# Optimization experiments

Hardware: AMD Instinct MI355X
Metric: run time of the kernel (lower is better)

The kernel has to match this reference:

```python
import jax, jax.numpy as jnp
import numpy as np
from jax import lax

NPOINT = 1024
FG_NSAMPLE = 512
TOPK = 2048
NSAMPLE = 32
RADIUS = 0.3
BN_EPS = 1e-5


def masked_fps(xyz, mask, n):
    """Farthest point sampling restricted to points where mask is True.
    xyz: [B,N,3] (grad-stopped), mask: [B,N] bool. Returns int32 [B,n] indices.
    Equivalent to running FPS on the masked subset starting at its first point."""
    xyz = lax.stop_gradient(xyz)

    def one(x, m):
        mind0 = jnp.where(m, jnp.float32(1e10), jnp.float32(-1.0))

        def body(i, carry):
            mind, idxs = carry
            sel = jnp.argmax(mind).astype(jnp.int32)
            d = jnp.sum((x - x[sel]) ** 2, axis=-1)
            mind = jnp.where(m, jnp.minimum(mind, d), jnp.float32(-1.0))
            return mind, idxs.at[i].set(sel)

        _, idxs = lax.fori_loop(0, n, body, (mind0, jnp.zeros((n,), jnp.int32)))
        return idxs

    return jax.vmap(one)(xyz, mask)


def ball_query(xyz, new_xyz, radius, nsample):
    """xyz: [B,N,3], new_xyz: [B,S,3] -> int32 [B,S,nsample] of first neighbors
    within radius (padded with the first found index, as in pointnet2 CUDA)."""
    x = lax.stop_gradient(xyz)
    q = lax.stop_gradient(new_xyz)
    d2 = jnp.sum((q[:, :, None, :] - x[:, None, :, :]) ** 2, axis=-1)  # [B,S,N]
    N = x.shape[1]
    ar = jnp.arange(N, dtype=jnp.float32)
    key = jnp.where(d2 <= radius * radius, ar, jnp.float32(N))
    neg_top, _ = lax.top_k(-key, nsample)  # smallest nsample indices
    idx = (-neg_top).astype(jnp.int32)
    first = idx[..., :1]
    idx = jnp.where(idx >= N, first, idx)
    return jnp.clip(idx, 0, N - 1)


def conv_bn_relu_2d(x, W, g, b):
    # x: [B,C,S,ns], W: [O,C]; 1x1 conv (no bias) + training-mode BN + ReLU
    y = jnp.einsum('oc,bcsn->bosn', W, x)
    mu = y.mean((0, 2, 3), keepdims=True)
    var = y.var((0, 2, 3), keepdims=True)
    y = (y - mu) * lax.rsqrt(var + BN_EPS) * g[None, :, None, None] + b[None, :, None, None]
    return jax.nn.relu(y)


def conv_bn_relu_1d(x, W, g, b):
    # x: [B,C,N]
    y = jnp.einsum('oc,bcn->bon', W, x)
    mu = y.mean((0, 2), keepdims=True)
    var = y.var((0, 2), keepdims=True)
    y = (y - mu) * lax.rsqrt(var + BN_EPS) * g[None, :, None] + b[None, :, None]
    return jax.nn.relu(y)


def batch_gather_points(x, idx):
    # x: [B,N,3], idx: [B,...] -> [B,...,3]
    return jax.vmap(lambda a, i: a[i])(x, idx)


def batch_gather_feats(f, idx):
    # f: [B,C,N], idx: [B,S,ns] -> [B,C,S,ns]
    return jax.vmap(lambda a, i: a[:, i])(f, idx)


def setup_inputs() -> dict:
    key = jax.random.key(0)
    ks = jax.random.split(key, 16)
    B, N, C = 4, 16384, 128
    s = 0.05
    return {
        'xyz': jax.random.uniform(ks[0], (B, N, 3), dtype=jnp.float32),
        'features': jax.random.normal(ks[1], (B, C, N), dtype=jnp.float32),
        # grouped shared MLP: (3+C)->128->128->256
        'w1': jax.random.normal(ks[2], (128, 131), dtype=jnp.float32) * s,
        'g1': jnp.ones((128,), jnp.float32), 'b1': jnp.zeros((128,), jnp.float32),
        'w2': jax.random.normal(ks[3], (128, 128), dtype=jnp.float32) * s,
        'g2': jnp.ones((128,), jnp.float32), 'b2': jnp.zeros((128,), jnp.float32),
        'w3': jax.random.normal(ks[4], (256, 128), dtype=jnp.float32) * s,
        'g3': jnp.ones((256,), jnp.float32), 'b3': jnp.zeros((256,), jnp.float32),
        # fbs mask MLP: C->64->2 (last layer plain conv with bias)
        'fw1': jax.random.normal(ks[5], (64, 128), dtype=jnp.float32) * s,
        'fg1': jnp.ones((64,), jnp.float32), 'fb1': jnp.zeros((64,), jnp.float32),
        'fw2': jax.random.normal(ks[6], (2, 64), dtype=jnp.float32) * s,
        'fbias2': jnp.zeros((2,), jnp.float32),
    }


def reference(xyz, features, w1, g1, b1, w2, g2, b2, w3, g3, b3, fw1, fg1, fb1, fw2, fbias2):
    B, N, _ = xyz.shape
    # --- FBS: foreground/background scoring ---
    h = conv_bn_relu_1d(features, fw1, fg1, fb1)                 # [B,64,N]
    mask_scores = jnp.einsum('oc,bcn->bon', fw2, h) + fbias2[None, :, None]  # [B,2,N]
    soft = jax.nn.softmax(mask_scores, axis=1)
    margin = soft[:, 1, :] - soft[:, 0, :]                        # [B,N]
    _, top_idx = lax.top_k(margin, TOPK)
    fg_mask = jnp.zeros((B, N), bool).at[jnp.arange(B)[:, None], top_idx].set(True)
    # --- mask-restricted FPS on foreground and background ---
    fg_idx = masked_fps(xyz, fg_mask, FG_NSAMPLE)                 # [B,512]
    bg_idx = masked_fps(xyz, ~fg_mask, NPOINT - FG_NSAMPLE)       # [B,512]
    indices = jnp.concatenate([fg_idx, bg_idx], axis=1)          # [B,npoint]
    new_xyz = batch_gather_points(xyz, indices)                   # [B,npoint,3]
    # --- ball query + grouping ---
    idx = ball_query(xyz, new_xyz, RADIUS, NSAMPLE)               # [B,S,ns]
    grouped_xyz = batch_gather_points(xyz, idx)                   # [B,S,ns,3]
    grouped_xyz = grouped_xyz - new_xyz[:, :, None, :]
    grouped_xyz = jnp.transpose(grouped_xyz, (0, 3, 1, 2))        # [B,3,S,ns]
    grouped_feats = batch_gather_feats(features, idx)             # [B,C,S,ns]
    x = jnp.concatenate([grouped_xyz, grouped_feats], axis=1)     # [B,3+C,S,ns]
    # --- shared MLP + max pool over neighbors ---
    x = conv_bn_relu_2d(x, w1, g1, b1)
    x = conv_bn_relu_2d(x, w2, g2, b2)
    x = conv_bn_relu_2d(x, w3, g3, b3)
    new_features = jnp.max(x, axis=-1)                            # [B,256,S]
    return new_xyz, new_features, indices, mask_scores
```

## Files before the change

kernel.cpp:

```cpp
#include <hip/hip_runtime.h>

#define BB 4
#define NPT 16384
#define CIN 128
#define SS 1024
#define NS 32
#define PP 131072
#define TOPKK 2048

typedef unsigned short u16;
typedef unsigned int u32;
typedef unsigned long long u64;
typedef float v2 __attribute__((ext_vector_type(2)));
typedef short bf16x8 __attribute__((ext_vector_type(8)));
typedef float f32x4 __attribute__((ext_vector_type(4)));

__device__ __forceinline__ float bf2f(u32 v){ return __uint_as_float(v << 16); }
__device__ __forceinline__ u16 f2bf(float f){
  u32 u = __float_as_uint(f);
  u32 r = (u + 0x7FFFu + ((u >> 16) & 1u)) >> 16;
  return (u16)r;
}
__device__ __forceinline__ u32 keyOf(float m){
  u32 u = __float_as_uint(m);
  return (u & 0x80000000u) ? ~u : (u | 0x80000000u);
}

__device__ __forceinline__ float wave_max_f32(float v){
  #define STEP(CTRL) { int o_ = __builtin_amdgcn_update_dpp(0, __float_as_int(v), CTRL, 0xf, 0xf, true); \
                       v = fmaxf(v, __int_as_float(o_)); }
  STEP(0x111) STEP(0x112) STEP(0x114) STEP(0x118)
  STEP(0x142) STEP(0x143)
  #undef STEP
  return __int_as_float(__builtin_amdgcn_readlane(__float_as_int(v), 63));
}

__device__ __forceinline__ float row_max16(float v){
  #define STEP(CTRL) { int o_ = __builtin_amdgcn_update_dpp(0, __float_as_int(v), CTRL, 0xf, 0xf, true); \
                       v = fmaxf(v, __int_as_float(o_)); }
  STEP(0x111) STEP(0x112) STEP(0x114) STEP(0x118)
  #undef STEP
  return v;
}

#define OFF_NEWXYZ 0ull
#define OFF_MARGIN 49152ull
#define OFF_FGMASK 311296ull
#define OFF_IDXNB  573440ull
#define OFF_MSTAT  1097728ull
#define OFF_SSA    1098240ull
#define OFF_WT0    1104384ull
#define OFF_W1B    1137152ull
#define OFF_W2B    1178112ull
#define OFF_W3B    1210880ull
#define OFF_MPART  1407488ull
#define OFF_CPART  2456064ull
#define OFF_REGB   10844672ull
#define OFF_REGA   44399104ull
#define WS_NEED    86342144ull

__global__ void k_prep(const float* __restrict__ w1, const float* __restrict__ w2,
                       const float* __restrict__ w3, const float* __restrict__ fw1,
                       float* __restrict__ wt0, u16* __restrict__ w1b, u16* __restrict__ w2b,
                       u16* __restrict__ w3b){
  int gt = blockIdx.x*blockDim.x + threadIdx.x;
  int gs = gridDim.x*blockDim.x;
  for (int i = gt; i < 128*64;  i += gs){ int k=i>>6, m=i&63;  wt0[i] = fw1[m*128+k]; }
  for (int i = gt; i < 128*160; i += gs){ int m=i/160, k=i-m*160; w1b[i] = (k<131)? f2bf(w1[m*131+k]) : (u16)0; }
  for (int i = gt; i < 128*128; i += gs){ w2b[i] = f2bf(w2[i]); }
  for (int i = gt; i < 256*128; i += gs){ w3b[i] = f2bf(w3[i]); }
}

__global__ __launch_bounds__(256) void k_gemm_mask(const float* __restrict__ Wt,
                                                   const float* __restrict__ feat,
                                                   float* __restrict__ y0,
                                                   double* __restrict__ mpart){
  __shared__ float As[32][64];
  __shared__ float Bs[32][64];
  int t = threadIdx.x, tx = t & 15, ty = t >> 4;
  int p0 = blockIdx.x * 64; int b = blockIdx.z;
  const float* X = feat + (size_t)b * CIN * NPT;
  float acc[4][4] = {};
  int e = t * 8, ka = e >> 6, ca = e & 63;
  for (int kc = 0; kc < 4; kc++){
    const float* wr = Wt + (size_t)(kc*32 + ka) * 64 + ca;
    float4 w0 = *(const float4*)wr;
    float4 w1v = *(const float4*)(wr + 4);
    const float* br = X + (size_t)(kc*32 + ka) * NPT + p0 + ca;
    float4 b0 = *(const float4*)br;
    float4 b1 = *(const float4*)(br + 4);
    __syncthreads();
    *(float4*)&As[ka][ca] = w0; *(float4*)&As[ka][ca+4] = w1v;
    *(float4*)&Bs[ka][ca] = b0; *(float4*)&Bs[ka][ca+4] = b1;
    __syncthreads();
    #pragma unroll
    for (int k = 0; k < 32; k++){
      float4 a = *(float4*)&As[k][ty*4];
      float4 bq = *(float4*)&Bs[k][tx*4];
      float av[4] = {a.x,a.y,a.z,a.w}; float bw[4] = {bq.x,bq.y,bq.z,bq.w};
      #pragma unroll
      for (int i = 0; i < 4; i++)
        #pragma unroll
        for (int j = 0; j < 4; j++) acc[i][j] = fmaf(av[i], bw[j], acc[i][j]);
    }
  }
  #pragma unroll
  for (int i = 0; i < 4; i++){
    int m = ty*4 + i;
    float4 v = make_float4(acc[i][0], acc[i][1], acc[i][2], acc[i][3]);
    *(float4*)(y0 + ((size_t)(b*64 + m)) * NPT + p0 + tx*4) = v;
  }
  __syncthreads();
  float* red = (float*)As;
  #pragma unroll
  for (int i = 0; i < 4; i++){
    float s = 0.f, q = 0.f;
    #pragma unroll
    for (int j = 0; j < 4; j++){ s += acc[i][j]; q += acc[i][j]*acc[i][j]; }
    red[((ty*4+i)*16 + tx)*2] = s; red[((ty*4+i)*16 + tx)*2 + 1] = q;
  }
  __syncthreads();
  if (t < 64){
    double s = 0.0, q = 0.0;
    for (int x = 0; x < 16; x++){ s += red[(t*16+x)*2]; q += red[(t*16+x)*2+1]; }
    int slot = b*256 + blockIdx.x;
    mpart[((size_t)t*1024 + slot)*2] = s;
    mpart[((size_t)t*1024 + slot)*2 + 1] = q;
  }
}

__global__ void k_mask_stats(const double* __restrict__ mpart, float* __restrict__ mstat){
  int t = threadIdx.x;
  double s = 0.0, q = 0.0;
  for (int i = 0; i < 1024; i++){ s += mpart[((size_t)t*1024 + i)*2]; q += mpart[((size_t)t*1024 + i)*2+1]; }
  double cnt = 65536.0;
  double mu = s/cnt; double var = q/cnt - mu*mu;
  mstat[t*2] = (float)mu; mstat[t*2+1] = 1.0f / sqrtf((float)var + 1e-5f);
}

__global__ __launch_bounds__(256) void k_scores(const float* __restrict__ y0, const float* __restrict__ mstat,
                                                const float* __restrict__ fg1, const float* __restrict__ fb1,
                                                const float* __restrict__ fw2, const float* __restrict__ fbias2,
                                                float* __restrict__ margin, float* __restrict__ out3){
  __shared__ float smu[64], srs[64], sg[64], sb[64], sw[128];
  int t = threadIdx.x; int b = blockIdx.y; int n = blockIdx.x*256 + t;
  if (t < 64){ smu[t] = mstat[t*2]; srs[t] = mstat[t*2+1]; sg[t] = fg1[t]; sb[t] = fb1[t]; }
  if (t < 128) sw[t] = fw2[t];
  __syncthreads();
  float a0 = 0.f, a1 = 0.f;
  const float* yb = y0 + (size_t)b*64*NPT + n;
  for (int o = 0; o < 64; o++){
    float y = yb[(size_t)o * NPT];
    float h = __fmul_rn(__fmul_rn(__fsub_rn(y, smu[o]), srs[o]), sg[o]);
    h = __fadd_rn(h, sb[o]);
    h = fmaxf(h, 0.f);
    a0 = fmaf(sw[o], h, a0);
    a1 = fmaf(sw[64+o], h, a1);
  }
  float s0 = __fadd_rn(a0, fbias2[0]);
  float s1 = __fadd_rn(a1, fbias2[1]);
  out3[(size_t)(b*2)*NPT + n] = s0;
  out3[(size_t)(b*2+1)*NPT + n] = s1;
  float m = fmaxf(s0, s1);
  float e0 = expf(__fsub_rn(s0, m));
  float e1 = expf(__fsub_rn(s1, m));
  float den = __fadd_rn(e0, e1);
  margin[b*NPT + n] = __fsub_rn(__fdiv_rn(e1, den), __fdiv_rn(e0, den));
}

__global__ __launch_bounds__(1024) void k_topk(const float* __restrict__ margin, u32* __restrict__ fgmask){
  int t = threadIdx.x; int b = blockIdx.x;
  int lane = t & 63, wv = t >> 6;
  const float* mg = margin + b*NPT; u32* fm = fgmask + b*NPT;
  __shared__ int hist[256];
  __shared__ int swt[2][16];
  __shared__ u32 s_bin; __shared__ int s_need;
  int need = TOPKK; u32 prefix = 0, kmask = 0;
  for (int r = 0; r < 4; r++){
    int shift = 24 - 8*r;
    if (t < 256) hist[t] = 0;
    __syncthreads();
    for (int j = 0; j < 16; j++){
      u32 key = keyOf(mg[j*1024 + t]);
      if ((key & kmask) == prefix) atomicAdd(&hist[(key >> shift) & 255], 1);
    }
    __syncthreads();
    if (t == 0){
      int cum = 0;
      for (int bin = 255; bin >= 0; bin--){
        int c = hist[bin];
        if (cum + c >= need){ s_bin = (u32)bin; s_need = need - cum; break; }
        cum += c;
      }
    }
    __syncthreads();
    prefix |= s_bin << shift; kmask |= 255u << shift; need = s_need;
    __syncthreads();
  }
  u32 T = prefix;
  int run = 0;
  for (int j = 0; j < 16; j++){
    int n = j*1024 + t;
    u32 key = keyOf(mg[n]);
    int eq = (key == T) ? 1 : 0;
    int gt = (key > T) ? 1 : 0;
    u64 bal = __ballot(eq != 0);
    int lexcl = __popcll(bal & ((1ull << lane) - 1ull));
    if (lane == 0) swt[j & 1][wv] = __popcll(bal);
    __syncthreads();
    int base = 0, tot = 0;
    #pragma unroll
    for (int w = 0; w < 16; w++){
      int c = swt[j & 1][w];
      tot += c;
      if (w < wv) base += c;
    }
    int flag = gt | (eq & ((run + base + lexcl) < need ? 1 : 0));
    fm[n] = (u32)flag;
    run += tot;
  }
}

__global__ __launch_bounds__(1024) void k_compact(const float* __restrict__ xyz, const u32* __restrict__ fgmask,
                                                  float* __restrict__ cx, float* __restrict__ cy,
                                                  float* __restrict__ cz, int* __restrict__ cg){
  int blk = blockIdx.x; int b = blk >> 1; int which = blk & 1;
  const float* xb = xyz + (size_t)b * NPT * 3;
  const u32* mb = fgmask + b*NPT;
  int t = threadIdx.x;
  __shared__ int sc[1024];
  u32 mloc = 0; int cnt = 0;
  int p0 = t*16;
  #pragma unroll
  for (int j = 0; j < 16; j++){
    u32 m = mb[p0+j];
    bool inc = which ? (m == 0u) : (m != 0u);
    mloc |= (inc ? 1u : 0u) << j; cnt += inc ? 1 : 0;
  }
  sc[t] = cnt; __syncthreads();
  for (int off = 1; off < 1024; off <<= 1){
    int v = (t >= off) ? sc[t-off] : 0;
    __syncthreads();
    sc[t] += v;
    __syncthreads();
  }
  int pos = sc[t] - cnt;
  int base = b*16384 + (which ? 2048 : 0);
  for (int j = 0; j < 16; j++){
    if ((mloc >> j) & 1u){
      int p = p0 + j;
      cx[base+pos] = xb[p*3]; cy[base+pos] = xb[p*3+1]; cz[base+pos] = xb[p*3+2];
      cg[base+pos] = p; pos++;
    }
  }
}

template<int NV>
__device__ __forceinline__ void fps_run(const float* __restrict__ cx, const float* __restrict__ cy,
                                        const float* __restrict__ cz, const int* __restrict__ cg,
                                        int b, int which,
                                        float* __restrict__ newxyz, float* __restrict__ out0,
                                        float* __restrict__ out2){
  #pragma clang fp contract(off)
  int t = threadIdx.x;
  __shared__ u64 slots[2][8];
  if (t < 16) ((u64*)slots)[t] = 0ull;
  v2 px[NV], py[NV], pz[NV], mind[NV];
  #pragma unroll
  for (int r = 0; r < NV; r++){
    int p0 = 1024*r + t, p1 = 1024*r + 512 + t;
    px[r].x = cx[p0]; px[r].y = cx[p1];
    py[r].x = cy[p0]; py[r].y = cy[p1];
    pz[r].x = cz[p0]; pz[r].y = cz[p1];
    mind[r].x = 1e10f; mind[r].y = 1e10f;
  }
  __syncthreads();
  float bv = 1e10f; int bi = t;
  for (int it = 0; it < 512; it++){
    float wall = wave_max_f32(bv);
    if (bv == wall){
      u64 key = ((u64)(it+1) << 46) | ((u64)keyOf(bv) << 14) | (u64)(16383 - bi);
      atomicMax((unsigned long long*)&slots[it & 1][t & 7], (unsigned long long)key);
    }
    __syncthreads();
    u64 k0 = slots[it & 1][0];
    #pragma unroll
    for (int i = 1; i < 8; i++){ u64 ki = slots[it & 1][i]; if (ki > k0) k0 = ki; }
    int sel = 16383 - (int)(k0 & 0x3FFFu);
    float xs = cx[sel], ys = cy[sel], zs = cz[sel];
    if (t == 0){
      int s = which*512 + it;
      out2[b*1024 + s] = (float)cg[sel];
      newxyz[(b*1024 + s)*3]   = xs;
      newxyz[(b*1024 + s)*3+1] = ys;
      newxyz[(b*1024 + s)*3+2] = zs;
      out0[(b*1024 + s)*3]   = xs;
      out0[(b*1024 + s)*3+1] = ys;
      out0[(b*1024 + s)*3+2] = zs;
    }
    v2 xs2; xs2.x = xs; xs2.y = xs;
    v2 ys2; ys2.x = ys; ys2.y = ys;
    v2 zs2; zs2.x = zs; zs2.y = zs;
    bv = -1.0f; bi = 16383;
    #pragma unroll
    for (int r = 0; r < NV; r++){
      v2 dx = px[r] - xs2;
      v2 dy = py[r] - ys2;
      v2 dz = pz[r] - zs2;
      v2 qx = dx * dx;
      v2 qy = dy * dy;
      v2 qz = dz * dz;
      v2 s1 = qx + qy;
      v2 d  = s1 + qz;
      float m0 = fminf(mind[r].x, d.x);
      float m1 = fminf(mind[r].y, d.y);
      mind[r].x = m0; mind[r].y = m1;
      if (m0 > bv){ bv = m0; bi = 1024*r + t; }
      if (m1 > bv){ bv = m1; bi = 1024*r + 512 + t; }
    }
  }
}

__global__ __launch_bounds__(512) void k_fps(const float* __restrict__ cx, const float* __restrict__ cy,
                                             const float* __restrict__ cz, const int* __restrict__ cg,
                                             float* __restrict__ newxyz, float* __restrict__ out0,
                                             float* __restrict__ out2){
  int b = blockIdx.x >> 1; int which = blockIdx.x & 1;
  int base = b*16384 + (which ? 2048 : 0);
  if (which) fps_run<14>(cx+base, cy+base, cz+base, cg+base, b, 1, newxyz, out0, out2);
  else       fps_run<2 >(cx+base, cy+base, cz+base, cg+base, b, 0, newxyz, out0, out2);
}

__global__ __launch_bounds__(256) void k_ball(const float* __restrict__ xyz, const float* __restrict__ newxyz,
                                              int* __restrict__ idxnb){
  int t = threadIdx.x; int lane = t & 63;
  int qid = blockIdx.x*4 + (t >> 6);
  int b = qid >> 10;
  const float* xb = xyz + (size_t)b * NPT * 3;
  float qx = newxyz[qid*3], qy = newxyz[qid*3+1], qz = newxyz[qid*3+2];
  int found = 0, first = -1;
  for (int base = 0; base < NPT; base += 64){
    int p = base + lane;
    float x = xb[p*3], y = xb[p*3+1], z = xb[p*3+2];
    float dx = __fsub_rn(qx, x), dy = __fsub_rn(qy, y), dz = __fsub_rn(qz, z);
    float d2 = __fadd_rn(__fadd_rn(__fmul_rn(dx,dx), __fmul_rn(dy,dy)), __fmul_rn(dz,dz));
    bool w = d2 <= 0.09f;
    u64 m = __ballot(w);
    if (first < 0 && m) first = base + __ffsll((unsigned long long)m) - 1;
    if (w){
      int pos = found + __popcll(m & ((1ull << lane) - 1ull));
      if (pos < NS) idxnb[(size_t)qid*NS + pos] = p;
    }
    found += __popcll(m);
    if (found >= NS) break;
  }
  if (first < 0) first = 0;
  if (lane < NS && lane >= found) idxnb[(size_t)qid*NS + lane] = first;
}

__global__ __launch_bounds__(256) void k_buildX(const float* __restrict__ xyz, const float* __restrict__ newxyz,
                                                const int* __restrict__ idxnb, const float* __restrict__ feat,
                                                u16* __restrict__ Xb2){
  int pos = blockIdx.x*256 + threadIdx.x;
  int b = pos >> 15; int r = pos & 32767; int s = r >> 5;
  int gi = idxnb[pos] & (NPT - 1);
  const float* xp = xyz + ((size_t)b*NPT + gi) * 3;
  const float* qp = newxyz + ((size_t)(b << 10) + s) * 3;
  float dxyz[3];
  #pragma unroll
  for (int c = 0; c < 3; c++) dxyz[c] = __fsub_rn(xp[c], qp[c]);
  const float* fb = feat + (size_t)b*CIN*NPT + gi;
  for (int g8 = 0; g8 < 20; g8++){
    u32 pk[4];
    #pragma unroll
    for (int i = 0; i < 4; i++){
      int c0 = g8*8 + 2*i, c1 = c0 + 1;
      float f0 = (c0 < 3) ? dxyz[c0] : ((c0 < 131) ? fb[(size_t)(c0-3)*NPT] : 0.f);
      float f1 = (c1 < 3) ? dxyz[c1] : ((c1 < 131) ? fb[(size_t)(c1-3)*NPT] : 0.f);
      pk[i] = (u32)f2bf(f0) | ((u32)f2bf(f1) << 16);
    }
    *(uint4*)(Xb2 + ((size_t)g8*PP + pos)*8) = make_uint4(pk[0], pk[1], pk[2], pk[3]);
  }
}

template<int NKS, int STORE>
__global__ __launch_bounds__(256) void k_mfma(const u16* __restrict__ Wb, int Kpad,
                                              const u16* __restrict__ Xp,
                                              u16* __restrict__ Yp, double* __restrict__ cpart){
  __shared__ float sred[4][16][16][2];
  int t = threadIdx.x;
  int w = t >> 6, lane = t & 63;
  int q = lane >> 4, c = lane & 15;
  int p0 = blockIdx.x * 64, m0 = blockIdx.y * 64;
  int m_w = m0 + w*16;
  f32x4 acc[4] = {{0.f,0.f,0.f,0.f},{0.f,0.f,0.f,0.f},{0.f,0.f,0.f,0.f},{0.f,0.f,0.f,0.f}};
  const u16* arow = Wb + (size_t)(m_w + c) * Kpad + q*8;
  #pragma unroll
  for (int ks = 0; ks < NKS; ks++){
    bf16x8 afrag = *(const bf16x8*)(arow + ks*32);
    #pragma unroll
    for (int pp = 0; pp < 4; pp++){
      int p = p0 + pp*16 + c;
      bf16x8 bfrag = *(const bf16x8*)(Xp + (((size_t)(ks*4 + q) * PP) + p) * 8);
      acc[pp] = __builtin_amdgcn_mfma_f32_16x16x32_bf16(afrag, bfrag, acc[pp], 0, 0, 0);
    }
  }
  #pragma unroll
  for (int reg = 0; reg < 4; reg++){
    float s = 0.f, sq = 0.f;
    #pragma unroll
    for (int pp = 0; pp < 4; pp++){ float v = acc[pp][reg]; s += v; sq += v*v; }
    sred[w][q*4+reg][c][0] = s; sred[w][q*4+reg][c][1] = sq;
  }
  if (STORE){
    int kgm = (m_w + q*4) >> 3;
    int j0 = (m_w + q*4) & 7;
    #pragma unroll
    for (int pp = 0; pp < 4; pp++){
      int p = p0 + pp*16 + c;
      ushort4 pk;
      pk.x = f2bf(acc[pp][0]); pk.y = f2bf(acc[pp][1]); pk.z = f2bf(acc[pp][2]); pk.w = f2bf(acc[pp][3]);
      *(ushort4*)(Yp + (((size_t)kgm * PP) + p) * 8 + j0) = pk;
    }
  }
  __syncthreads();
  if (t < 64){
    int ww = t >> 4, ml = t & 15;
    double s = 0.0, qq = 0.0;
    for (int cc = 0; cc < 16; cc++){ s += sred[ww][ml][cc][0]; qq += sred[ww][ml][cc][1]; }
    cpart[((size_t)(m0 + t) * 2048 + blockIdx.x)*2] = s;
    cpart[((size_t)(m0 + t) * 2048 + blockIdx.x)*2 + 1] = qq;
  }
}

__global__ __launch_bounds__(256) void k_mfma_pool(const u16* __restrict__ Wb,
                                                   const u16* __restrict__ Xp,
                                                   const float2* __restrict__ ss2,
                                                   float* __restrict__ out1){
  int t = threadIdx.x;
  int w = t >> 6, lane = t & 63;
  int q = lane >> 4, c = lane & 15;
  int p0 = blockIdx.x * 64, m0 = blockIdx.y * 64;
  int m_w = m0 + w*16;
  f32x4 acc[4] = {{0.f,0.f,0.f,0.f},{0.f,0.f,0.f,0.f},{0.f,0.f,0.f,0.f},{0.f,0.f,0.f,0.f}};
  const u16* arow = Wb + (size_t)(m_w + c) * 128 + q*8;
  #pragma unroll
  for (int ks = 0; ks < 4; ks++){
    bf16x8 afrag = *(const bf16x8*)(arow + ks*32);
    #pragma unroll
    for (int pp = 0; pp < 4; pp++){
      int p = p0 + pp*16 + c;
      bf16x8 bfrag = *(const bf16x8*)(Xp + (((size_t)(ks*4 + q) * PP) + p) * 8);
      acc[pp] = __builtin_amdgcn_mfma_f32_16x16x32_bf16(afrag, bfrag, acc[pp], 0, 0, 0);
    }
  }
  int qid0 = blockIdx.x*2;
  #pragma unroll
  for (int reg = 0; reg < 4; reg++){
    int m = m_w + q*4 + reg;
    float2 af = ss2[m];
    float x0 = fmaxf(0.f, fmaf(acc[0][reg], af.x, af.y));
    float x1 = fmaxf(0.f, fmaf(acc[1][reg], af.x, af.y));
    float x2 = fmaxf(0.f, fmaf(acc[2][reg], af.x, af.y));
    float x3 = fmaxf(0.f, fmaf(acc[3][reg], af.x, af.y));
    float v0 = row_max16(fmaxf(x0, x1));
    float v1 = row_max16(fmaxf(x2, x3));
    if (c == 15){
      int qa = qid0, qb = qid0 + 1;
      out1[((size_t)(qa >> 10) << 18) + (size_t)m*1024 + (qa & 1023)] = v0;
      out1[((size_t)(qb >> 10) << 18) + (size_t)m*1024 + (qb & 1023)] = v1;
    }
  }
}

__global__ __launch_bounds__(256) void k_stats_conv(const double* __restrict__ cpart,
                                                    const float* __restrict__ g, const float* __restrict__ bt,
                                                    float2* __restrict__ ssv){
  __shared__ double rs_[256], rq_[256];
  int ch = blockIdx.x, t = threadIdx.x;
  double s = 0.0, q = 0.0;
  for (int i = t; i < 2048; i += 256){ s += cpart[((size_t)ch*2048 + i)*2]; q += cpart[((size_t)ch*2048 + i)*2+1]; }
  rs_[t] = s; rq_[t] = q; __syncthreads();
  for (int off = 128; off; off >>= 1){
    if (t < off){ rs_[t] += rs_[t+off]; rq_[t] += rq_[t+off]; }
    __syncthreads();
  }
  if (t == 0){
    double cnt = (double)PP;
    double mu = rs_[0]/cnt; double var = rq_[0]/cnt - mu*mu;
    float rsf = 1.0f / sqrtf((float)var + 1e-5f);
    double rsd = (double)rsf;
    double gd = (double)g[ch]; double bd = (double)bt[ch];
    ssv[ch] = make_float2((float)(rsd*gd), (float)(bd - mu*rsd*gd));
  }
}

__global__ __launch_bounds__(256) void k_affine(u16* __restrict__ y, const float2* __restrict__ aff){
  int tid = blockIdx.x*256 + threadIdx.x;
  int kg = tid >> 17; int p = tid & (PP - 1);
  uint4* ptr = (uint4*)(y + (((size_t)kg*PP) + p)*8);
  uint4 u = *ptr;
  u32 us[4] = {u.x, u.y, u.z, u.w};
  u32 outp[4];
  #pragma unroll
  for (int i = 0; i < 4; i++){
    float2 a0 = aff[kg*8 + 2*i], a1 = aff[kg*8 + 2*i + 1];
    float v0 = fmaxf(0.f, fmaf(bf2f(us[i] & 0xFFFFu), a0.x, a0.y));
    float v1 = fmaxf(0.f, fmaf(bf2f(us[i] >> 16),     a1.x, a1.y));
    outp[i] = (u32)f2bf(v0) | ((u32)f2bf(v1) << 16);
  }
  *ptr = make_uint4(outp[0], outp[1], outp[2], outp[3]);
}

extern "C" void kernel_launch(void* const* d_in, const int* in_sizes, int n_in,
                              void* d_out, int out_size, void* d_ws, size_t ws_size,
                              hipStream_t stream){
  (void)in_sizes; (void)n_in; (void)out_size;
  if (ws_size < WS_NEED) return;
  const float* xyz    = (const float*)d_in[0];
  const float* feat   = (const float*)d_in[1];
  const float* w1     = (const float*)d_in[2];
  const float* g1     = (const float*)d_in[3];
  const float* b1     = (const float*)d_in[4];
  const float* w2     = (const float*)d_in[5];
  const float* g2     = (const float*)d_in[6];
  const float* b2     = (const float*)d_in[7];
  const float* w3     = (const float*)d_in[8];
  const float* g3     = (const float*)d_in[9];
  const float* b3     = (const float*)d_in[10];
  const float* fw1    = (const float*)d_in[11];
  const float* fg1    = (const float*)d_in[12];
  const float* fb1    = (const float*)d_in[13];
  const float* fw2    = (const float*)d_in[14];
  const float* fbias2 = (const float*)d_in[15];

  char* ws = (char*)d_ws;
  float*  newxyz = (float*)(ws + OFF_NEWXYZ);
  float*  margin = (float*)(ws + OFF_MARGIN);
  u32*    fgmask = (u32*)(ws + OFF_FGMASK);
  int*    idxnb  = (int*)(ws + OFF_IDXNB);
  float*  mstat  = (float*)(ws + OFF_MSTAT);
  float2* ss0    = (float2*)(ws + OFF_SSA);
  float2* ss1    = ss0 + 128;
  float2* ss2    = ss0 + 256;
  float*  wt0    = (float*)(ws + OFF_WT0);
  u16*    w1b    = (u16*)(ws + OFF_W1B);
  u16*    w2b    = (u16*)(ws + OFF_W2B);
  u16*    w3b    = (u16*)(ws + OFF_W3B);
  double* mpart  = (double*)(ws + OFF_MPART);
  double* cpart  = (double*)(ws + OFF_CPART);
  u16*    Y1p    = (u16*)(ws + OFF_REGB);
  float*  y0     = (float*)(ws + OFF_REGA);
  float*  cx     = (float*)(ws + OFF_REGA);
  float*  cy     = cx + 4*16384;
  float*  cz     = cy + 4*16384;
  int*    cg     = (int*)(cz + 4*16384);
  u16*    Xb2    = (u16*)(ws + OFF_REGA);
  u16*    Y2p    = (u16*)(ws + OFF_REGA);

  float* out  = (float*)d_out;
  float* out0 = out;
  float* out1 = out + 12288;
  float* out2 = out + 1060864;
  float* out3 = out + 1064960;

  k_prep<<<dim3(256), dim3(256), 0, stream>>>(w1, w2, w3, fw1, wt0, w1b, w2b, w3b);
  k_gemm_mask<<<dim3(256,1,4), dim3(256), 0, stream>>>(wt0, feat, y0, mpart);
  k_mask_stats<<<dim3(1), dim3(64), 0, stream>>>(mpart, mstat);
  k_scores<<<dim3(64,4), dim3(256), 0, stream>>>(y0, mstat, fg1, fb1, fw2, fbias2, margin, out3);
  k_topk<<<dim3(4), dim3(1024), 0, stream>>>(margin, fgmask);
  k_compact<<<dim3(8), dim3(1024), 0, stream>>>(xyz, fgmask, cx, cy, cz, cg);
  k_fps<<<dim3(8), dim3(512), 0, stream>>>(cx, cy, cz, cg, newxyz, out0, out2);
  k_ball<<<dim3(1024), dim3(256), 0, stream>>>(xyz, newxyz, idxnb);
  k_buildX<<<dim3(512), dim3(256), 0, stream>>>(xyz, newxyz, idxnb, feat, Xb2);
  k_mfma<5,1><<<dim3(2048,2), dim3(256), 0, stream>>>(w1b, 160, Xb2, Y1p, cpart);
  k_stats_conv<<<dim3(128), dim3(256), 0, stream>>>(cpart, g1, b1, ss0);
  k_affine<<<dim3(8192), dim3(256), 0, stream>>>(Y1p, ss0);
  k_mfma<4,1><<<dim3(2048,2), dim3(256), 0, stream>>>(w2b, 128, Y1p, Y2p, cpart);
  k_stats_conv<<<dim3(128), dim3(256), 0, stream>>>(cpart, g2, b2, ss1);
  k_affine<<<dim3(8192), dim3(256), 0, stream>>>(Y2p, ss1);
  k_mfma<4,0><<<dim3(2048,4), dim3(256), 0, stream>>>(w3b, 128, Y2p, (u16*)nullptr, cpart);
  k_stats_conv<<<dim3(256), dim3(256), 0, stream>>>(cpart, g3, b3, ss2);
  k_mfma_pool<<<dim3(2048,4), dim3(256), 0, stream>>>(w3b, Y2p, ss2, out1);
}
```

Measured before the change: 1.233 ms.

## Pre-transpose features to point-major bf16 rows and simplify FPS argmax

Adds a kernel that transposes the features into a point-major bf16 buffer padded to 160 channels, so the grouping kernel can read each neighbour's feature row with contiguous 16-byte loads. Before, it made strided per-channel fp32 gathers. The FPS loop also drops the wave-level max reduction and has every thread issue a shared-memory atomicMax directly. The transpose adds a full pass over the features plus one extra launch. Having all threads hit the atomics increases contention on the shared slots in every one of the 512 serial iterations.

```diff
diff --git a/kernel.cpp b/kernel.cpp
--- a/kernel.cpp
+++ b/kernel.cpp
@@ -24,15 +24,6 @@
 __device__ __forceinline__ u32 keyOf(float m){
   u32 u = __float_as_uint(m);
   return (u & 0x80000000u) ? ~u : (u | 0x80000000u);
-}
-
-__device__ __forceinline__ float wave_max_f32(float v){
-  #define STEP(CTRL) { int o_ = __builtin_amdgcn_update_dpp(0, __float_as_int(v), CTRL, 0xf, 0xf, true); \
-                       v = fmaxf(v, __int_as_float(o_)); }
-  STEP(0x111) STEP(0x112) STEP(0x114) STEP(0x118)
-  STEP(0x142) STEP(0x143)
-  #undef STEP
-  return __int_as_float(__builtin_amdgcn_readlane(__float_as_int(v), 63));
 }
 
 __device__ __forceinline__ float row_max16(float v){
@@ -69,6 +60,23 @@
   for (int i = gt; i < 128*160; i += gs){ int m=i/160, k=i-m*160; w1b[i] = (k<131)? f2bf(w1[m*131+k]) : (u16)0; }
   for (int i = gt; i < 128*128; i += gs){ w2b[i] = f2bf(w2[i]); }
   for (int i = gt; i < 256*128; i += gs){ w3b[i] = f2bf(w3[i]); }
+}
+
+__global__ __launch_bounds__(256) void k_prepT(const float* __restrict__ feat, u16* __restrict__ featT2){
+  __shared__ u16 tile[128][66];
+  int b = blockIdx.y; int n0 = blockIdx.x * 64;
+  int t = threadIdx.x;
+  #pragma unroll
+  for (int it = 0; it < 32; it++){
+    int idx = it*256 + t; int c = idx >> 6, nn = idx & 63;
+    tile[c][nn] = f2bf(feat[((size_t)b*CIN + c)*NPT + n0 + nn]);
+  }
+  __syncthreads();
+  for (int it = 0; it < 40; it++){
+    int idx = it*256 + t; int nn = idx / 160; int c = idx - nn*160;
+    u16 v = (c >= 3 && c < 131) ? tile[c-3][nn] : (u16)0;
+    featT2[((size_t)(b*NPT + n0 + nn))*160 + c] = v;
+  }
 }
 
 __global__ __launch_bounds__(256) void k_gemm_mask(const float* __restrict__ Wt,
@@ -277,11 +285,8 @@
   __syncthreads();
   float bv = 1e10f; int bi = t;
   for (int it = 0; it < 512; it++){
-    float wall = wave_max_f32(bv);
-    if (bv == wall){
-      u64 key = ((u64)(it+1) << 46) | ((u64)keyOf(bv) << 14) | (u64)(16383 - bi);
-      atomicMax((unsigned long long*)&slots[it & 1][t & 7], (unsigned long long)key);
-    }
+    u64 key = ((u64)(it+1) << 46) | ((u64)keyOf(bv) << 14) | (u64)(16383 - bi);
+    atomicMax((unsigned long long*)&slots[it & 1][t & 7], (unsigned long long)key);
     __syncthreads();
     u64 k0 = slots[it & 1][0];
     #pragma unroll
@@ -359,27 +364,25 @@
 }
 
 __global__ __launch_bounds__(256) void k_buildX(const float* __restrict__ xyz, const float* __restrict__ newxyz,
-                                                const int* __restrict__ idxnb, const float* __restrict__ feat,
+                                                const int* __restrict__ idxnb, const u16* __restrict__ featT2,
                                                 u16* __restrict__ Xb2){
   int pos = blockIdx.x*256 + threadIdx.x;
   int b = pos >> 15; int r = pos & 32767; int s = r >> 5;
   int gi = idxnb[pos] & (NPT - 1);
   const float* xp = xyz + ((size_t)b*NPT + gi) * 3;
   const float* qp = newxyz + ((size_t)(b << 10) + s) * 3;
-  float dxyz[3];
-  #pragma unroll
-  for (int c = 0; c < 3; c++) dxyz[c] = __fsub_rn(xp[c], qp[c]);
-  const float* fb = feat + (size_t)b*CIN*NPT + gi;
-  for (int g8 = 0; g8 < 20; g8++){
-    u32 pk[4];
-    #pragma unroll
-    for (int i = 0; i < 4; i++){
-      int c0 = g8*8 + 2*i, c1 = c0 + 1;
-      float f0 = (c0 < 3) ? dxyz[c0] : ((c0 < 131) ? fb[(size_t)(c0-3)*NPT] : 0.f);
-      float f1 = (c1 < 3) ? dxyz[c1] : ((c1 < 131) ? fb[(size_t)(c1-3)*NPT] : 0.f);
-      pk[i] = (u32)f2bf(f0) | ((u32)f2bf(f1) << 16);
-    }
-    *(uint4*)(Xb2 + ((size_t)g8*PP + pos)*8) = make_uint4(pk[0], pk[1], pk[2], pk[3]);
+  u16 d0 = f2bf(__fsub_rn(xp[0], qp[0]));
+  u16 d1 = f2bf(__fsub_rn(xp[1], qp[1]));
+  u16 d2 = f2bf(__fsub_rn(xp[2], qp[2]));
+  const uint4* row = (const uint4*)(featT2 + (size_t)(b*NPT + gi) * 160);
+  #pragma unroll
+  for (int kg = 0; kg < 20; kg++){
+    uint4 u = row[kg];
+    if (kg == 0){
+      u.x = (u32)d0 | ((u32)d1 << 16);
+      u.y = (u.y & 0xFFFF0000u) | (u32)d2;
+    }
+    *(uint4*)(Xb2 + ((size_t)kg*PP + pos)*8) = u;
   }
 }
 
@@ -549,6 +552,7 @@
   u16*    w3b    = (u16*)(ws + OFF_W3B);
   double* mpart  = (double*)(ws + OFF_MPART);
   double* cpart  = (double*)(ws + OFF_CPART);
+  u16*    featT2 = (u16*)(ws + OFF_REGB);
   u16*    Y1p    = (u16*)(ws + OFF_REGB);
   float*  y0     = (float*)(ws + OFF_REGA);
   float*  cx     = (float*)(ws + OFF_REGA);
@@ -565,6 +569,7 @@
   float* out3 = out + 1064960;
 
   k_prep<<<dim3(256), dim3(256), 0, stream>>>(w1, w2, w3, fw1, wt0, w1b, w2b, w3b);
+  k_prepT<<<dim3(256,4), dim3(256), 0, stream>>>(feat, featT2);
   k_gemm_mask<<<dim3(256,1,4), dim3(256), 0, stream>>>(wt0, feat, y0, mpart);
   k_mask_stats<<<dim3(1), dim3(64), 0, stream>>>(mpart, mstat);
   k_scores<<<dim3(64,4), dim3(256), 0, stream>>>(y0, mstat, fg1, fb1, fw2, fbias2, margin, out3);
@@ -572,7 +577,7 @@
   k_compact<<<dim3(8), dim3(1024), 0, stream>>>(xyz, fgmask, cx, cy, cz, cg);
   k_fps<<<dim3(8), dim3(512), 0, stream>>>(cx, cy, cz, cg, newxyz, out0, out2);
   k_ball<<<dim3(1024), dim3(256), 0, stream>>>(xyz, newxyz, idxnb);
-  k_buildX<<<dim3(512), dim3(256), 0, stream>>>(xyz, newxyz, idxnb, feat, Xb2);
+  k_buildX<<<dim3(512), dim3(256), 0, stream>>>(xyz, newxyz, idxnb, featT2, Xb2);
   k_mfma<5,1><<<dim3(2048,2), dim3(256), 0, stream>>>(w1b, 160, Xb2, Y1p, cpart);
   k_stats_conv<<<dim3(128), dim3(256), 0, stream>>>(cpart, g1, b1, ss0);
   k_affine<<<dim3(8192), dim3(256), 0, stream>>>(Y1p, ss0);
```

New measurement: 1.169 ms. 5.2% less time.
